# Optimization experiments

Hardware: AMD Instinct MI355X
Metric: run time of the kernel (lower is better)

Reference implementation:

```python
import jax, jax.numpy as jnp
import numpy as np

B, T, C = 8, 2048, 1024   # batch, seq_len, n_embd
H = 128                   # head_size

def setup_inputs() -> dict:
    key = jax.random.key(0)
    kx, kk, kq, kv = jax.random.split(key, 4)
    scale = 1.0 / np.sqrt(C)
    return {
        "x": jax.random.normal(kx, (B, T, C), dtype=jnp.float32),
        "Wk": jax.random.normal(kk, (C, H), dtype=jnp.float32) * scale,
        "Wq": jax.random.normal(kq, (C, H), dtype=jnp.float32) * scale,
        "Wv": jax.random.normal(kv, (C, H), dtype=jnp.float32) * scale,
    }

def reference(x, Wk, Wq, Wv):
    # k,q,v: [B,T,H]
    k = x @ Wk
    q = x @ Wq
    v = x @ Wv
    # NOTE: original scales by C**-0.5 (n_embd), not head_size**-0.5
    wei = jnp.einsum("bth,bsh->bts", q, k) * (x.shape[-1] ** -0.5)  # [B,T,T]
    wei = jax.nn.softmax(wei, axis=-1)  # no causal mask in the source module
    # dropout = 0.0 -> identity
    out = jnp.einsum("bts,bsh->bth", wei, v)  # [B,T,H]
    return out
```

## Files before the change

### kernel.cpp

```cpp
#include <hip/hip_runtime.h>
#include <hip/hip_bf16.h>
#include <stdint.h>
#include <stddef.h>

#define NB 8
#define NT 2048
#define NC 1024
#define NH 128

typedef float f32x4 __attribute__((ext_vector_type(4)));
typedef short bf16x8 __attribute__((ext_vector_type(8)));
typedef short bf16x4 __attribute__((ext_vector_type(4)));

__device__ __forceinline__ unsigned short f2bf(float f) {
    union { float f; uint32_t u; } v; v.f = f;
    uint32_t u = v.u;
    u += 0x7fffu + ((u >> 16) & 1u);
    return (unsigned short)(u >> 16);
}

__device__ __forceinline__ void gld16(const void* gp, void* lp) {
    __builtin_amdgcn_global_load_lds(
        (const __attribute__((address_space(1))) unsigned int*)gp,
        (__attribute__((address_space(3))) unsigned int*)lp, 16, 0, 0);
}


__global__ __launch_bounds__(256) void cast_w_kernel(const float* __restrict__ Wq,
                                                     const float* __restrict__ Wk,
                                                     const float* __restrict__ Wv,
                                                     unsigned short* __restrict__ Wtf) {
    int gid  = blockIdx.x * 256 + threadIdx.x;
    int lane = gid & 63;
    int fs   = gid >> 6;
    int kb   = fs & 31;
    int g    = fs >> 5;
    int w    = g >> 3;
    int g16  = g & 7;
    int quad = lane >> 4;
    int l16  = lane & 15;
    const float* src = (w == 0) ? Wq : ((w == 1) ? Wk : Wv);
    int n = g16 * 16 + l16;
    bf16x8 o;
#pragma unroll
    for (int j = 0; j < 8; ++j)
        o[j] = (short)f2bf(src[(size_t)(kb * 32 + quad * 8 + j) * 128 + n]);
    *(bf16x8*)(Wtf + (size_t)gid * 8) = o;
}

#define CS2 392

__global__ __launch_bounds__(512, 2) void proj_kernel(const float* __restrict__ x,
                                                      const unsigned short* __restrict__ Wtf,
                                                      unsigned short* __restrict__ Qf,
                                                      unsigned short* __restrict__ Kf,
                                                      unsigned short* __restrict__ Vf) {
    __shared__ __align__(16) unsigned short wbuf[4][24 * 512];
    __shared__ __align__(16) unsigned short abuf[2][64 * 128];

    const int tid  = threadIdx.x;
    const int wave = tid >> 6;
    const int lane = tid & 63;
    const int quad = lane >> 4;
    const int l16  = lane & 15;
    const int bidx = blockIdx.x;
    const int rowbase = bidx * 64;
    const int b    = bidx >> 5;
    const int mh   = wave & 1;
    const int nq   = wave >> 1;

    const int arow = wave * 8 + (lane >> 3);
    const float* axp = x + (size_t)(rowbase + arow) * NC;
    const int aswz = (arow & 7) << 3;
    const int rswz = (l16 & 7) << 3;

    float4 aS[2][4];
    f32x4 acc0[6] = {};
    f32x4 acc1[6] = {};

#define STAGE(KB, BI) { _Pragma("unroll") \
    for (int i_ = 0; i_ < 3; ++i_) { \
        const int g_ = wave * 3 + i_; \
        gld16(Wtf + ((size_t)(g_ * 32 + (KB)) * 512) + lane * 8, &wbuf[BI][g_ * 512]); } }

#define LOADA(C, S) { _Pragma("unroll") \
    for (int i_ = 0; i_ < 4; ++i_) \
        aS[S][i_] = *(const float4*)(axp + (C) * 128 + i_ * 32 + (lane & 7) * 4); }

#define DSWRITE(C, S) { _Pragma("unroll") \
    for (int i_ = 0; i_ < 4; ++i_) { \
        bf16x4 t_; \
        t_[0] = (short)f2bf(aS[S][i_].x); t_[1] = (short)f2bf(aS[S][i_].y); \
        t_[2] = (short)f2bf(aS[S][i_].z); t_[3] = (short)f2bf(aS[S][i_].w); \
        *(bf16x4*)(&abuf[(C) & 1][arow * 128 + ((i_ * 32 + (lane & 7) * 4) ^ aswz)]) = t_; } }

#define BARW(N) { asm volatile("s_waitcnt vmcnt(" #N ") lgkmcnt(0)" ::: "memory"); \
                  __builtin_amdgcn_s_barrier(); }

#define TICK(K, CUR) { \
    const unsigned short* ab_ = abuf[((K) >> 2) & 1]; \
    const int t2_ = ((K) & 3) * 32 + quad * 8; \
    bf16x8 af0 = *(const bf16x8*)(ab_ + (mh * 32 + l16) * 128 + (t2_ ^ rswz)); \
    bf16x8 af1 = *(const bf16x8*)(ab_ + (mh * 32 + 16 + l16) * 128 + (t2_ ^ rswz)); \
    _Pragma("unroll") \
    for (int i_ = 0; i_ < 6; ++i_) { \
        bf16x8 wf_ = *(const bf16x8*)(&wbuf[CUR][(nq * 6 + i_) * 512 + lane * 8]); \
        acc0[i_] = __builtin_amdgcn_mfma_f32_16x16x32_bf16(af0, wf_, acc0[i_], 0, 0, 0); \
        acc1[i_] = __builtin_amdgcn_mfma_f32_16x16x32_bf16(af1, wf_, acc1[i_], 0, 0, 0); } }

    LOADA(0, 0); LOADA(1, 1);
    STAGE(0, 0); STAGE(1, 1); STAGE(2, 2);
    asm volatile("s_waitcnt vmcnt(13)" ::: "memory");
    DSWRITE(0, 0);
    BARW(6);

    for (int c = 0; c < 6; ++c) {
        const int k0 = c * 4;
        LOADA(c + 2, c & 1);
        STAGE(k0 + 3, 3); TICK(k0 + 0, 0); BARW(10);
        STAGE(k0 + 4, 0); TICK(k0 + 1, 1); BARW(10);
        STAGE(k0 + 5, 1); TICK(k0 + 2, 2); BARW(6);
        STAGE(k0 + 6, 2); TICK(k0 + 3, 3); DSWRITE(c + 1, (c + 1) & 1); BARW(6);
    }
    STAGE(27, 3); TICK(24, 0); BARW(6);
    STAGE(28, 0); TICK(25, 1); BARW(6);
    STAGE(29, 1); TICK(26, 2); BARW(6);
    STAGE(30, 2); TICK(27, 3); DSWRITE(7, 1); BARW(6);
    STAGE(31, 3); TICK(28, 0); BARW(6);
    TICK(29, 1); BARW(3);
    TICK(30, 2); BARW(0);
    TICK(31, 3);
    asm volatile("s_waitcnt vmcnt(0) lgkmcnt(0)" ::: "memory");
    __builtin_amdgcn_s_barrier();

    unsigned short* cs = (unsigned short*)wbuf;
#pragma unroll
    for (int i = 0; i < 6; ++i) {
#pragma unroll
        for (int r = 0; r < 4; ++r) {
            cs[(mh * 32 +  0 + quad * 4 + r) * CS2 + nq * 96 + i * 16 + l16] = f2bf(acc0[i][r]);
            cs[(mh * 32 + 16 + quad * 4 + r) * CS2 + nq * 96 + i * 16 + l16] = f2bf(acc1[i][r]);
        }
    }
    __syncthreads();

    const int ibase = (rowbase & (NT - 1)) >> 4;
    const int tc    = (rowbase & (NT - 1)) >> 5;
    unsigned short* qdst = Qf + (size_t)b * (NT * NH);
    unsigned short* kdst = Kf + (size_t)b * (NT * NH);
    unsigned short* vdst = Vf + (size_t)b * (NT * NH);

#pragma unroll
    for (int j = 0; j < 6; ++j) {
        const int s = wave * 6 + j;
        if (s < 32) {
            const int isK = s >> 4;
            const int t   = s & 15;
            const int m   = t >> 2;
            const int ks  = t & 3;
            unsigned short* dst = isK ? kdst : qdst;
            bf16x8 v = *(const bf16x8*)(&cs[(m * 16 + l16) * CS2 + isK * 128 + ks * 32 + quad * 8]);
            *(bf16x8*)(dst + ((size_t)((ibase + m) * 4 + ks) * 64 + lane) * 8) = v;
        } else {
            const int vv = s - 32;
            const int nt = vv >> 1;
            const int cc = vv & 1;
            bf16x8 v;
#pragma unroll
            for (int jj = 0; jj < 8; ++jj)
                v[jj] = (short)cs[(cc * 32 + quad * 8 + jj) * CS2 + 256 + nt * 16 + l16];
            *(bf16x8*)(vdst + ((size_t)(nt * 64 + tc + cc) * 64 + lane) * 8) = v;
        }
    }

#undef TICK
#undef BARW
#undef DSWRITE
#undef LOADA
#undef STAGE
}

#define KBUF(BI) (smem + (BI) * 16384)
#define VBUF(BI) (smem + 32768 + (BI) * 16384)

__global__ __launch_bounds__(512, 1) void attn_kernel(const unsigned short* __restrict__ Qf,
                                                      const unsigned short* __restrict__ Kf,
                                                      const unsigned short* __restrict__ Vf,
                                                      float* __restrict__ out) {
    __shared__ __align__(16) unsigned short smem[4 * 32 * 512];
    __shared__ __align__(16) unsigned short p_all[8][32 * 40];
    __shared__ float sl[8][32];

    const int tid  = threadIdx.x;
    const int wave = tid >> 6;
    const int lane = tid & 63;
    const int quad = lane >> 4;
    const int l16  = lane & 15;
    const int bid  = blockIdx.x;
    const int b    = bid & 7;
    const int iqg  = bid >> 3;
    const int mh   = wave & 1;
    const int kq   = wave >> 1;

    const unsigned short* qfp = Qf + (size_t)b * (NT * NH);
    const unsigned short* kfp = Kf + (size_t)b * (NT * NH);
    const unsigned short* vfp = Vf + (size_t)b * (NT * NH);
    unsigned short* p_w = p_all[wave];

    const int iq0 = iqg * 4 + mh * 2;
    bf16x8 qf0[4], qf1[4];
#pragma unroll
    for (int ks = 0; ks < 4; ++ks) {
        qf0[ks] = *(const bf16x8*)(qfp + ((size_t)((iq0 + 0) * 4 + ks) * 64 + lane) * 8);
        qf1[ks] = *(const bf16x8*)(qfp + ((size_t)((iq0 + 1) * 4 + ks) * 64 + lane) * 8);
    }

    auto stage = [&](int j, int bi) {
#pragma unroll
        for (int i = 0; i < 8; ++i) {
            const int fid = wave * 8 + i;
            if (fid < 32) {
                gld16(kfp + ((size_t)(j * 32 + fid) * 512) + lane * 8, KBUF(bi) + fid * 512);
            } else {
                const int s  = fid - 32;
                const int nt = s >> 2;
                const int t4 = s & 3;
                gld16(vfp + ((size_t)(nt * 64 + j * 4 + t4) * 512) + lane * 8, VBUF(bi) + s * 512);
            }
        }
    };

    stage(0, 0);
    __syncthreads();

    f32x4 O0[8] = {}, O1[8] = {};
    float lsum0[4] = {0.f, 0.f, 0.f, 0.f};
    float lsum1[4] = {0.f, 0.f, 0.f, 0.f};
    const float scl2 = 0.03125f * 1.44269504088896340736f;

    for (int j = 0; j < 16; ++j) {
        const int cur = j & 1;
        if (j < 15) stage(j + 1, cur ^ 1);
        const unsigned short* kb = KBUF(cur);
        const unsigned short* vb = VBUF(cur);

        f32x4 S00 = {}, S01 = {}, S10 = {}, S11 = {};
#pragma unroll
        for (int ks = 0; ks < 4; ++ks) {
            bf16x8 kf0 = *(const bf16x8*)(kb + ((kq * 2 + 0) * 4 + ks) * 512 + lane * 8);
            bf16x8 kf1 = *(const bf16x8*)(kb + ((kq * 2 + 1) * 4 + ks) * 512 + lane * 8);
            S00 = __builtin_amdgcn_mfma_f32_16x16x32_bf16(qf0[ks], kf0, S00, 0, 0, 0);
            S01 = __builtin_amdgcn_mfma_f32_16x16x32_bf16(qf0[ks], kf1, S01, 0, 0, 0);
            S10 = __builtin_amdgcn_mfma_f32_16x16x32_bf16(qf1[ks], kf0, S10, 0, 0, 0);
            S11 = __builtin_amdgcn_mfma_f32_16x16x32_bf16(qf1[ks], kf1, S11, 0, 0, 0);
        }

#pragma unroll
        for (int r = 0; r < 4; ++r) {
            float p00 = __builtin_amdgcn_exp2f(S00[r] * scl2);
            float p01 = __builtin_amdgcn_exp2f(S01[r] * scl2);
            float p10 = __builtin_amdgcn_exp2f(S10[r] * scl2);
            float p11 = __builtin_amdgcn_exp2f(S11[r] * scl2);
            lsum0[r] += p00 + p01;
            lsum1[r] += p10 + p11;
            p_w[(quad * 4 + r) * 40 + l16]           = f2bf(p00);
            p_w[(quad * 4 + r) * 40 + 16 + l16]      = f2bf(p01);
            p_w[(16 + quad * 4 + r) * 40 + l16]      = f2bf(p10);
            p_w[(16 + quad * 4 + r) * 40 + 16 + l16] = f2bf(p11);
        }

        bf16x8 pf0 = *(const bf16x8*)(&p_w[l16 * 40 + quad * 8]);
        bf16x8 pf1 = *(const bf16x8*)(&p_w[(16 + l16) * 40 + quad * 8]);
#pragma unroll
        for (int nt = 0; nt < 8; ++nt) {
            bf16x8 vf = *(const bf16x8*)(vb + (nt * 4 + kq) * 512 + lane * 8);
            O0[nt] = __builtin_amdgcn_mfma_f32_16x16x32_bf16(pf0, vf, O0[nt], 0, 0, 0);
            O1[nt] = __builtin_amdgcn_mfma_f32_16x16x32_bf16(pf1, vf, O1[nt], 0, 0, 0);
        }

        __syncthreads();
    }

#pragma unroll
    for (int msk = 1; msk <= 8; msk <<= 1) {
#pragma unroll
        for (int r = 0; r < 4; ++r) {
            lsum0[r] += __shfl_xor(lsum0[r], msk, 64);
            lsum1[r] += __shfl_xor(lsum1[r], msk, 64);
        }
    }
    if (l16 == 0) {
#pragma unroll
        for (int r = 0; r < 4; ++r) {
            sl[wave][quad * 4 + r]      = lsum0[r];
            sl[wave][16 + quad * 4 + r] = lsum1[r];
        }
    }

    float* od = (float*)smem;
    if (kq > 0) {
        float* myod = od + (size_t)((kq - 1) * 2 + mh) * 32 * 132;
#pragma unroll
        for (int nt = 0; nt < 8; ++nt) {
#pragma unroll
            for (int r = 0; r < 4; ++r) {
                myod[(quad * 4 + r) * 132 + nt * 16 + l16]      = O0[nt][r];
                myod[(16 + quad * 4 + r) * 132 + nt * 16 + l16] = O1[nt][r];
            }
        }
    }
    __syncthreads();

    if (kq == 0) {
        float inv0[4], inv1[4];
#pragma unroll
        for (int r = 0; r < 4; ++r) {
            inv0[r] = 1.0f / (sl[mh][quad * 4 + r] + sl[2 + mh][quad * 4 + r] +
                              sl[4 + mh][quad * 4 + r] + sl[6 + mh][quad * 4 + r]);
            inv1[r] = 1.0f / (sl[mh][16 + quad * 4 + r] + sl[2 + mh][16 + quad * 4 + r] +
                              sl[4 + mh][16 + quad * 4 + r] + sl[6 + mh][16 + quad * 4 + r]);
        }
        float* orow = out + ((size_t)b * NT + iqg * 64 + mh * 32) * NH;
#pragma unroll
        for (int nt = 0; nt < 8; ++nt) {
#pragma unroll
            for (int r = 0; r < 4; ++r) {
                float v0 = O0[nt][r];
                float v1 = O1[nt][r];
#pragma unroll
                for (int w6 = 0; w6 < 3; ++w6) {
                    v0 += od[((size_t)(w6 * 2 + mh) * 32 + quad * 4 + r) * 132 + nt * 16 + l16];
                    v1 += od[((size_t)(w6 * 2 + mh) * 32 + 16 + quad * 4 + r) * 132 + nt * 16 + l16];
                }
                orow[(quad * 4 + r) * NH + nt * 16 + l16]      = v0 * inv0[r];
                orow[(16 + quad * 4 + r) * NH + nt * 16 + l16] = v1 * inv1[r];
            }
        }
    }
}

#undef KBUF
#undef VBUF

extern "C" void kernel_launch(void* const* d_in, const int* in_sizes, int n_in,
                              void* d_out, int out_size, void* d_ws, size_t ws_size,
                              hipStream_t stream) {
    const float* x  = (const float*)d_in[0];
    const float* Wk = (const float*)d_in[1];
    const float* Wq = (const float*)d_in[2];
    const float* Wv = (const float*)d_in[3];
    float* out = (float*)d_out;

    char* ws = (char*)d_ws;
    unsigned short* Qf  = (unsigned short*)(ws);
    unsigned short* Kf  = (unsigned short*)(ws + 4194304);
    unsigned short* Vf  = (unsigned short*)(ws + 8388608);
    unsigned short* Wtf = (unsigned short*)(ws + 12582912);

    cast_w_kernel<<<192, 256, 0, stream>>>(Wq, Wk, Wv, Wtf);
    proj_kernel<<<256, 512, 0, stream>>>(x, Wtf, Qf, Kf, Vf);
    attn_kernel<<<256, 512, 0, stream>>>(Qf, Kf, Vf, out);
}
```

Before: 148.9 us.

## Split projection into smaller 32-row blocks with double-buffered weight staging

The projection kernel now uses 256-thread blocks that each handle 32 rows, launched as 512 blocks instead of 256 blocks of 512 threads handling 64 rows. Weight staging in LDS drops from a 4-deep to a 2-deep ring, and the hand-tuned vmcnt barriers are replaced with plain __syncthreads. The output scatter is reorganised to match the new wave layout. The aim is more blocks for better CU coverage and lower LDS use per block. In exchange, each weight tile is loaded by twice as many blocks, and the shallower pipeline with full syncs exposes more load latency.

```diff
diff --git a/kernel.cpp b/kernel.cpp
--- a/kernel.cpp
+++ b/kernel.cpp
@@ -50,13 +50,13 @@
 
 #define CS2 392
 
-__global__ __launch_bounds__(512, 2) void proj_kernel(const float* __restrict__ x,
+__global__ __launch_bounds__(256, 2) void proj_kernel(const float* __restrict__ x,
                                                       const unsigned short* __restrict__ Wtf,
                                                       unsigned short* __restrict__ Qf,
                                                       unsigned short* __restrict__ Kf,
                                                       unsigned short* __restrict__ Vf) {
-    __shared__ __align__(16) unsigned short wbuf[4][24 * 512];
-    __shared__ __align__(16) unsigned short abuf[2][64 * 128];
+    __shared__ __align__(16) unsigned short wbuf[2][24 * 512];
+    __shared__ __align__(16) unsigned short abuf[2][32 * 128];
 
     const int tid  = threadIdx.x;
     const int wave = tid >> 6;
@@ -64,12 +64,10 @@
     const int quad = lane >> 4;
     const int l16  = lane & 15;
     const int bidx = blockIdx.x;
-    const int rowbase = bidx * 64;
-    const int b    = bidx >> 5;
-    const int mh   = wave & 1;
-    const int nq   = wave >> 1;
-
-    const int arow = wave * 8 + (lane >> 3);
+    const int rowbase = bidx * 32;
+    const int b    = bidx >> 6;
+
+    const int arow = tid >> 3;
     const float* axp = x + (size_t)(rowbase + arow) * NC;
     const int aswz = (arow & 7) << 3;
     const int rswz = (l16 & 7) << 3;
@@ -79,67 +77,60 @@
     f32x4 acc1[6] = {};
 
 #define STAGE(KB, BI) { _Pragma("unroll") \
-    for (int i_ = 0; i_ < 3; ++i_) { \
-        const int g_ = wave * 3 + i_; \
+    for (int i_ = 0; i_ < 6; ++i_) { \
+        const int g_ = wave * 6 + i_; \
         gld16(Wtf + ((size_t)(g_ * 32 + (KB)) * 512) + lane * 8, &wbuf[BI][g_ * 512]); } }
 
 #define LOADA(C, S) { _Pragma("unroll") \
     for (int i_ = 0; i_ < 4; ++i_) \
-        aS[S][i_] = *(const float4*)(axp + (C) * 128 + i_ * 32 + (lane & 7) * 4); }
+        aS[S][i_] = *(const float4*)(axp + (C) * 128 + i_ * 32 + (tid & 7) * 4); }
 
 #define DSWRITE(C, S) { _Pragma("unroll") \
     for (int i_ = 0; i_ < 4; ++i_) { \
         bf16x4 t_; \
         t_[0] = (short)f2bf(aS[S][i_].x); t_[1] = (short)f2bf(aS[S][i_].y); \
         t_[2] = (short)f2bf(aS[S][i_].z); t_[3] = (short)f2bf(aS[S][i_].w); \
-        *(bf16x4*)(&abuf[(C) & 1][arow * 128 + ((i_ * 32 + (lane & 7) * 4) ^ aswz)]) = t_; } }
-
-#define BARW(N) { asm volatile("s_waitcnt vmcnt(" #N ") lgkmcnt(0)" ::: "memory"); \
-                  __builtin_amdgcn_s_barrier(); }
-
-#define TICK(K, CUR) { \
-    const unsigned short* ab_ = abuf[((K) >> 2) & 1]; \
+        *(bf16x4*)(&abuf[(C) & 1][arow * 128 + ((i_ * 32 + (tid & 7) * 4) ^ aswz)]) = t_; } }
+
+#define TICK(K, AB, CUR) { \
     const int t2_ = ((K) & 3) * 32 + quad * 8; \
-    bf16x8 af0 = *(const bf16x8*)(ab_ + (mh * 32 + l16) * 128 + (t2_ ^ rswz)); \
-    bf16x8 af1 = *(const bf16x8*)(ab_ + (mh * 32 + 16 + l16) * 128 + (t2_ ^ rswz)); \
+    bf16x8 af0 = *(const bf16x8*)(&abuf[AB][l16 * 128 + (t2_ ^ rswz)]); \
+    bf16x8 af1 = *(const bf16x8*)(&abuf[AB][(16 + l16) * 128 + (t2_ ^ rswz)]); \
     _Pragma("unroll") \
     for (int i_ = 0; i_ < 6; ++i_) { \
-        bf16x8 wf_ = *(const bf16x8*)(&wbuf[CUR][(nq * 6 + i_) * 512 + lane * 8]); \
+        bf16x8 wf_ = *(const bf16x8*)(&wbuf[CUR][(wave * 6 + i_) * 512 + lane * 8]); \
         acc0[i_] = __builtin_amdgcn_mfma_f32_16x16x32_bf16(af0, wf_, acc0[i_], 0, 0, 0); \
         acc1[i_] = __builtin_amdgcn_mfma_f32_16x16x32_bf16(af1, wf_, acc1[i_], 0, 0, 0); } }
 
-    LOADA(0, 0); LOADA(1, 1);
-    STAGE(0, 0); STAGE(1, 1); STAGE(2, 2);
-    asm volatile("s_waitcnt vmcnt(13)" ::: "memory");
+#define CHUNK(C, SN, DO_LA, DO_DW) { \
+    STAGE(4*(C)+1, 1); if (DO_LA) { LOADA((C)+1, SN); } TICK(4*(C)+0, (C)&1, 0); __syncthreads(); \
+    STAGE(4*(C)+2, 0); TICK(4*(C)+1, (C)&1, 1); __syncthreads(); \
+    STAGE(4*(C)+3, 1); TICK(4*(C)+2, (C)&1, 0); __syncthreads(); \
+    if ((C) < 7) { STAGE(4*(C)+4, 0); } TICK(4*(C)+3, (C)&1, 1); \
+    if (DO_DW) { DSWRITE((C)+1, SN); } __syncthreads(); }
+
+    LOADA(0, 0);
+    STAGE(0, 0);
+    asm volatile("s_waitcnt vmcnt(6)" ::: "memory");
     DSWRITE(0, 0);
-    BARW(6);
-
-    for (int c = 0; c < 6; ++c) {
-        const int k0 = c * 4;
-        LOADA(c + 2, c & 1);
-        STAGE(k0 + 3, 3); TICK(k0 + 0, 0); BARW(10);
-        STAGE(k0 + 4, 0); TICK(k0 + 1, 1); BARW(10);
-        STAGE(k0 + 5, 1); TICK(k0 + 2, 2); BARW(6);
-        STAGE(k0 + 6, 2); TICK(k0 + 3, 3); DSWRITE(c + 1, (c + 1) & 1); BARW(6);
-    }
-    STAGE(27, 3); TICK(24, 0); BARW(6);
-    STAGE(28, 0); TICK(25, 1); BARW(6);
-    STAGE(29, 1); TICK(26, 2); BARW(6);
-    STAGE(30, 2); TICK(27, 3); DSWRITE(7, 1); BARW(6);
-    STAGE(31, 3); TICK(28, 0); BARW(6);
-    TICK(29, 1); BARW(3);
-    TICK(30, 2); BARW(0);
-    TICK(31, 3);
-    asm volatile("s_waitcnt vmcnt(0) lgkmcnt(0)" ::: "memory");
-    __builtin_amdgcn_s_barrier();
+    __syncthreads();
+
+    CHUNK(0, 1, 1, 1);
+    CHUNK(1, 0, 1, 1);
+    CHUNK(2, 1, 1, 1);
+    CHUNK(3, 0, 1, 1);
+    CHUNK(4, 1, 1, 1);
+    CHUNK(5, 0, 1, 1);
+    CHUNK(6, 1, 1, 1);
+    CHUNK(7, 0, 0, 0);
 
     unsigned short* cs = (unsigned short*)wbuf;
 #pragma unroll
     for (int i = 0; i < 6; ++i) {
 #pragma unroll
         for (int r = 0; r < 4; ++r) {
-            cs[(mh * 32 +  0 + quad * 4 + r) * CS2 + nq * 96 + i * 16 + l16] = f2bf(acc0[i][r]);
-            cs[(mh * 32 + 16 + quad * 4 + r) * CS2 + nq * 96 + i * 16 + l16] = f2bf(acc1[i][r]);
+            cs[(quad * 4 + r) * CS2 + wave * 96 + i * 16 + l16]        = f2bf(acc0[i][r]);
+            cs[(16 + quad * 4 + r) * CS2 + wave * 96 + i * 16 + l16]   = f2bf(acc1[i][r]);
         }
     }
     __syncthreads();
@@ -150,31 +141,30 @@
     unsigned short* kdst = Kf + (size_t)b * (NT * NH);
     unsigned short* vdst = Vf + (size_t)b * (NT * NH);
 
-#pragma unroll
-    for (int j = 0; j < 6; ++j) {
-        const int s = wave * 6 + j;
-        if (s < 32) {
-            const int isK = s >> 4;
-            const int t   = s & 15;
-            const int m   = t >> 2;
-            const int ks  = t & 3;
-            unsigned short* dst = isK ? kdst : qdst;
-            bf16x8 v = *(const bf16x8*)(&cs[(m * 16 + l16) * CS2 + isK * 128 + ks * 32 + quad * 8]);
-            *(bf16x8*)(dst + ((size_t)((ibase + m) * 4 + ks) * 64 + lane) * 8) = v;
-        } else {
-            const int vv = s - 32;
-            const int nt = vv >> 1;
-            const int cc = vv & 1;
-            bf16x8 v;
-#pragma unroll
-            for (int jj = 0; jj < 8; ++jj)
-                v[jj] = (short)cs[(cc * 32 + quad * 8 + jj) * CS2 + 256 + nt * 16 + l16];
-            *(bf16x8*)(vdst + ((size_t)(nt * 64 + tc + cc) * 64 + lane) * 8) = v;
-        }
-    }
-
+    {
+        const int mq   = wave & 1;
+        const int isK  = wave >> 1;
+        unsigned short* dst = isK ? kdst : qdst;
+        const int off = isK * 128;
+        const int iqt = ibase + mq;
+#pragma unroll
+        for (int ks = 0; ks < 4; ++ks) {
+            bf16x8 v = *(const bf16x8*)(&cs[(mq * 16 + l16) * CS2 + off + ks * 32 + quad * 8]);
+            *(bf16x8*)(dst + ((size_t)(iqt * 4 + ks) * 64 + lane) * 8) = v;
+        }
+    }
+#pragma unroll
+    for (int i = 0; i < 2; ++i) {
+        const int nt = wave * 2 + i;
+        bf16x8 v;
+#pragma unroll
+        for (int j = 0; j < 8; ++j)
+            v[j] = (short)cs[(quad * 8 + j) * CS2 + 256 + nt * 16 + l16];
+        *(bf16x8*)(vdst + ((size_t)(nt * 64 + tc) * 64 + lane) * 8) = v;
+    }
+
+#undef CHUNK
 #undef TICK
-#undef BARW
 #undef DSWRITE
 #undef LOADA
 #undef STAGE
@@ -358,6 +348,6 @@
     unsigned short* Wtf = (unsigned short*)(ws + 12582912);
 
     cast_w_kernel<<<192, 256, 0, stream>>>(Wq, Wk, Wv, Wtf);
-    proj_kernel<<<256, 512, 0, stream>>>(x, Wtf, Qf, Kf, Vf);
+    proj_kernel<<<512, 256, 0, stream>>>(x, Wtf, Qf, Kf, Vf);
     attn_kernel<<<256, 512, 0, stream>>>(Qf, Kf, Vf, out);
 }
```

New measurement: 147.3 us. No clear change (-1.1%).

## Triple-buffer smaller KV tiles and split waves across key and head halves

Applied to the files above, without the earlier changes.

The attention kernel now streams 16-key K/V tiles through a three-slot shared-memory ring, prefetching two tiles ahead with explicit vmcnt waits instead of double-buffering 32-key tiles. Waves are regrouped so each pair shares a P tile: waves split the key chunk in two and the V head dimension in two, which halves per-wave O accumulators and shrinks the final cross-wave reduction to one partner. The goal is to hide more global-load latency and cut register pressure and reduction traffic. In exchange there are twice as many loop iterations and two workgroup barriers per iteration, because P is now shared across waves.

```diff
diff --git a/kernel.cpp b/kernel.cpp
--- a/kernel.cpp
+++ b/kernel.cpp
@@ -180,15 +180,15 @@
 #undef STAGE
 }
 
-#define KBUF(BI) (smem + (BI) * 16384)
-#define VBUF(BI) (smem + 32768 + (BI) * 16384)
+#define AKBUF(BI) (smem + (size_t)(BI) * 8192)
+#define AVBUF(BI) (smem + 24576 + (size_t)(BI) * 8192)
 
 __global__ __launch_bounds__(512, 1) void attn_kernel(const unsigned short* __restrict__ Qf,
                                                       const unsigned short* __restrict__ Kf,
                                                       const unsigned short* __restrict__ Vf,
                                                       float* __restrict__ out) {
-    __shared__ __align__(16) unsigned short smem[4 * 32 * 512];
-    __shared__ __align__(16) unsigned short p_all[8][32 * 40];
+    __shared__ __align__(16) unsigned short smem[6 * 16 * 512];
+    __shared__ __align__(16) unsigned short p_grp[4][32 * 40];
     __shared__ float sl[8][32];
 
     const int tid  = threadIdx.x;
@@ -200,12 +200,14 @@
     const int b    = bid & 7;
     const int iqg  = bid >> 3;
     const int mh   = wave & 1;
-    const int kq   = wave >> 1;
+    const int kh   = (wave >> 1) & 1;
+    const int nh   = wave >> 2;
+    const int kq   = kh * 2 + nh;
 
     const unsigned short* qfp = Qf + (size_t)b * (NT * NH);
     const unsigned short* kfp = Kf + (size_t)b * (NT * NH);
     const unsigned short* vfp = Vf + (size_t)b * (NT * NH);
-    unsigned short* p_w = p_all[wave];
+    unsigned short* pg = p_grp[mh * 2 + kh];
 
     const int iq0 = iqg * 4 + mh * 2;
     bf16x8 qf0[4], qf1[4];
@@ -217,68 +219,73 @@
 
     auto stage = [&](int j, int bi) {
 #pragma unroll
-        for (int i = 0; i < 8; ++i) {
-            const int fid = wave * 8 + i;
-            if (fid < 32) {
-                gld16(kfp + ((size_t)(j * 32 + fid) * 512) + lane * 8, KBUF(bi) + fid * 512);
+        for (int i = 0; i < 4; ++i) {
+            const int fid = wave * 4 + i;
+            if (fid < 16) {
+                gld16(kfp + ((size_t)(j * 16 + fid) * 512) + lane * 8, AKBUF(bi) + fid * 512);
             } else {
-                const int s  = fid - 32;
-                const int nt = s >> 2;
-                const int t4 = s & 3;
-                gld16(vfp + ((size_t)(nt * 64 + j * 4 + t4) * 512) + lane * 8, VBUF(bi) + s * 512);
+                const int s  = fid - 16;
+                const int nt = s >> 1;
+                const int c  = s & 1;
+                gld16(vfp + ((size_t)(nt * 64 + j * 2 + c) * 512) + lane * 8, AVBUF(bi) + s * 512);
             }
         }
     };
 
     stage(0, 0);
-    __syncthreads();
-
-    f32x4 O0[8] = {}, O1[8] = {};
+    stage(1, 1);
+    asm volatile("s_waitcnt vmcnt(4)" ::: "memory");
+    __builtin_amdgcn_s_barrier();
+
+    f32x4 O0[4] = {}, O1[4] = {};
     float lsum0[4] = {0.f, 0.f, 0.f, 0.f};
     float lsum1[4] = {0.f, 0.f, 0.f, 0.f};
     const float scl2 = 0.03125f * 1.44269504088896340736f;
 
-    for (int j = 0; j < 16; ++j) {
-        const int cur = j & 1;
-        if (j < 15) stage(j + 1, cur ^ 1);
-        const unsigned short* kb = KBUF(cur);
-        const unsigned short* vb = VBUF(cur);
-
-        f32x4 S00 = {}, S01 = {}, S10 = {}, S11 = {};
+    for (int j = 0; j < 32; ++j) {
+        const int cur = j - (j / 3) * 3;
+        const int nxt = (j + 2 >= 3 * ((j + 2) / 3)) ? (j + 2) - 3 * ((j + 2) / 3) : 0;
+        if (j < 30) stage(j + 2, nxt);
+        const unsigned short* kb = AKBUF(cur);
+        const unsigned short* vb = AVBUF(cur);
+
+        f32x4 S0 = {}, S1 = {};
 #pragma unroll
         for (int ks = 0; ks < 4; ++ks) {
-            bf16x8 kf0 = *(const bf16x8*)(kb + ((kq * 2 + 0) * 4 + ks) * 512 + lane * 8);
-            bf16x8 kf1 = *(const bf16x8*)(kb + ((kq * 2 + 1) * 4 + ks) * 512 + lane * 8);
-            S00 = __builtin_amdgcn_mfma_f32_16x16x32_bf16(qf0[ks], kf0, S00, 0, 0, 0);
-            S01 = __builtin_amdgcn_mfma_f32_16x16x32_bf16(qf0[ks], kf1, S01, 0, 0, 0);
-            S10 = __builtin_amdgcn_mfma_f32_16x16x32_bf16(qf1[ks], kf0, S10, 0, 0, 0);
-            S11 = __builtin_amdgcn_mfma_f32_16x16x32_bf16(qf1[ks], kf1, S11, 0, 0, 0);
-        }
-
-#pragma unroll
-        for (int r = 0; r < 4; ++r) {
-            float p00 = __builtin_amdgcn_exp2f(S00[r] * scl2);
-            float p01 = __builtin_amdgcn_exp2f(S01[r] * scl2);
-            float p10 = __builtin_amdgcn_exp2f(S10[r] * scl2);
-            float p11 = __builtin_amdgcn_exp2f(S11[r] * scl2);
-            lsum0[r] += p00 + p01;
-            lsum1[r] += p10 + p11;
-            p_w[(quad * 4 + r) * 40 + l16]           = f2bf(p00);
-            p_w[(quad * 4 + r) * 40 + 16 + l16]      = f2bf(p01);
-            p_w[(16 + quad * 4 + r) * 40 + l16]      = f2bf(p10);
-            p_w[(16 + quad * 4 + r) * 40 + 16 + l16] = f2bf(p11);
-        }
-
-        bf16x8 pf0 = *(const bf16x8*)(&p_w[l16 * 40 + quad * 8]);
-        bf16x8 pf1 = *(const bf16x8*)(&p_w[(16 + l16) * 40 + quad * 8]);
-#pragma unroll
-        for (int nt = 0; nt < 8; ++nt) {
-            bf16x8 vf = *(const bf16x8*)(vb + (nt * 4 + kq) * 512 + lane * 8);
-            O0[nt] = __builtin_amdgcn_mfma_f32_16x16x32_bf16(pf0, vf, O0[nt], 0, 0, 0);
-            O1[nt] = __builtin_amdgcn_mfma_f32_16x16x32_bf16(pf1, vf, O1[nt], 0, 0, 0);
-        }
-
-        __syncthreads();
+            bf16x8 kf = *(const bf16x8*)(kb + (kq * 4 + ks) * 512 + lane * 8);
+            S0 = __builtin_amdgcn_mfma_f32_16x16x32_bf16(qf0[ks], kf, S0, 0, 0, 0);
+            S1 = __builtin_amdgcn_mfma_f32_16x16x32_bf16(qf1[ks], kf, S1, 0, 0, 0);
+        }
+
+#pragma unroll
+        for (int r = 0; r < 4; ++r) {
+            float p0 = __builtin_amdgcn_exp2f(S0[r] * scl2);
+            float p1 = __builtin_amdgcn_exp2f(S1[r] * scl2);
+            lsum0[r] += p0;
+            lsum1[r] += p1;
+            pg[(quad * 4 + r) * 40 + nh * 16 + l16]        = f2bf(p0);
+            pg[(16 + quad * 4 + r) * 40 + nh * 16 + l16]   = f2bf(p1);
+        }
+
+        asm volatile("s_waitcnt lgkmcnt(0)" ::: "memory");
+        __builtin_amdgcn_s_barrier();
+
+        bf16x8 pf0 = *(const bf16x8*)(&pg[l16 * 40 + quad * 8]);
+        bf16x8 pf1 = *(const bf16x8*)(&pg[(16 + l16) * 40 + quad * 8]);
+#pragma unroll
+        for (int i = 0; i < 4; ++i) {
+            const int nt = nh * 4 + i;
+            bf16x8 vf = *(const bf16x8*)(vb + (nt * 2 + kh) * 512 + lane * 8);
+            O0[i] = __builtin_amdgcn_mfma_f32_16x16x32_bf16(pf0, vf, O0[i], 0, 0, 0);
+            O1[i] = __builtin_amdgcn_mfma_f32_16x16x32_bf16(pf1, vf, O1[i], 0, 0, 0);
+        }
+
+        if (j < 30) {
+            asm volatile("s_waitcnt vmcnt(4) lgkmcnt(0)" ::: "memory");
+        } else {
+            asm volatile("s_waitcnt vmcnt(0) lgkmcnt(0)" ::: "memory");
+        }
+        __builtin_amdgcn_s_barrier();
     }
 
 #pragma unroll
@@ -296,22 +303,24 @@
             sl[wave][16 + quad * 4 + r] = lsum1[r];
         }
     }
+    __syncthreads();
 
     float* od = (float*)smem;
-    if (kq > 0) {
-        float* myod = od + (size_t)((kq - 1) * 2 + mh) * 32 * 132;
-#pragma unroll
-        for (int nt = 0; nt < 8; ++nt) {
+    const int g = nh * 2 + mh;
+    if (kh == 1) {
+        float* myod = od + (size_t)g * 32 * 68;
+#pragma unroll
+        for (int i = 0; i < 4; ++i) {
 #pragma unroll
             for (int r = 0; r < 4; ++r) {
-                myod[(quad * 4 + r) * 132 + nt * 16 + l16]      = O0[nt][r];
-                myod[(16 + quad * 4 + r) * 132 + nt * 16 + l16] = O1[nt][r];
+                myod[(quad * 4 + r) * 68 + i * 16 + l16]      = O0[i][r];
+                myod[(16 + quad * 4 + r) * 68 + i * 16 + l16] = O1[i][r];
             }
         }
     }
     __syncthreads();
 
-    if (kq == 0) {
+    if (kh == 0) {
         float inv0[4], inv1[4];
 #pragma unroll
         for (int r = 0; r < 4; ++r) {
@@ -320,27 +329,23 @@
             inv1[r] = 1.0f / (sl[mh][16 + quad * 4 + r] + sl[2 + mh][16 + quad * 4 + r] +
                               sl[4 + mh][16 + quad * 4 + r] + sl[6 + mh][16 + quad * 4 + r]);
         }
-        float* orow = out + ((size_t)b * NT + iqg * 64 + mh * 32) * NH;
-#pragma unroll
-        for (int nt = 0; nt < 8; ++nt) {
+        const float* pod = od + (size_t)g * 32 * 68;
+        float* orow = out + ((size_t)b * NT + iqg * 64 + mh * 32) * NH + nh * 64;
+#pragma unroll
+        for (int i = 0; i < 4; ++i) {
 #pragma unroll
             for (int r = 0; r < 4; ++r) {
-                float v0 = O0[nt][r];
-                float v1 = O1[nt][r];
-#pragma unroll
-                for (int w6 = 0; w6 < 3; ++w6) {
-                    v0 += od[((size_t)(w6 * 2 + mh) * 32 + quad * 4 + r) * 132 + nt * 16 + l16];
-                    v1 += od[((size_t)(w6 * 2 + mh) * 32 + 16 + quad * 4 + r) * 132 + nt * 16 + l16];
-                }
-                orow[(quad * 4 + r) * NH + nt * 16 + l16]      = v0 * inv0[r];
-                orow[(16 + quad * 4 + r) * NH + nt * 16 + l16] = v1 * inv1[r];
+                float v0 = O0[i][r] + pod[(quad * 4 + r) * 68 + i * 16 + l16];
+                float v1 = O1[i][r] + pod[(16 + quad * 4 + r) * 68 + i * 16 + l16];
+                orow[(quad * 4 + r) * NH + i * 16 + l16]      = v0 * inv0[r];
+                orow[(16 + quad * 4 + r) * NH + i * 16 + l16] = v1 * inv1[r];
             }
         }
     }
 }
 
-#undef KBUF
-#undef VBUF
+#undef AKBUF
+#undef AVBUF
 
 extern "C" void kernel_launch(void* const* d_in, const int* in_sizes, int n_in,
                               void* d_out, int out_size, void* d_ws, size_t ws_size,
```

Measured after the change: 155.4 us. +4.4%, slower.
